# Optimization experiments

Measured on AMD Instinct MI355X. Metric: run time of the kernel, lower is better.

## Reference

```python
import jax, jax.numpy as jnp
import numpy as np
from jax import lax

B, N, C, D = 8, 512, 37, 2048          # frames, rois/frame, classes (incl. bg), feat dim
SCORE_THR = 0.1
NMS_THR = 0.4
BBOX_STDS = np.array([0.1, 0.1, 0.2, 0.2], dtype=np.float32)


def setup_inputs() -> dict:
    key = jax.random.key(0)
    k1, k2, k3, k4, k5, k6 = jax.random.split(key, 6)
    # rois: [batch_idx, x1, y1, x2, y2] in a 600x1000 image
    x1 = jax.random.uniform(k1, (B, N)) * 900.0
    y1 = jax.random.uniform(k2, (B, N)) * 500.0
    w = jax.random.uniform(k3, (B, N)) * 120.0 + 8.0
    h = jax.random.uniform(k4, (B, N)) * 120.0 + 8.0
    bidx = jnp.broadcast_to(jnp.arange(B, dtype=jnp.float32)[:, None], (B, N))
    rois = jnp.stack([bidx, x1, y1, x1 + w, y1 + h], axis=-1)  # [B,N,5]
    bbox_pred = jax.random.normal(k5, (B, N, 4 * C)) * 0.5
    scores = jax.nn.softmax(jax.random.normal(k6, (B, N, C)) * 2.0, axis=-1)
    im_info = jnp.tile(jnp.array([[600.0, 1000.0, 1.0]], dtype=jnp.float32), (B, 1))
    roi_features = jax.random.normal(jax.random.fold_in(key, 7), (B, N, D))
    return {"rois": rois, "bbox_pred": bbox_pred, "scores": scores,
            "im_info": im_info, "roi_features": roi_features}


def _iou_matrix(b):
    # b: [N,4] -> [N,N] pairwise IoU (torchvision nms convention, no +1)
    area = (b[:, 2] - b[:, 0]) * (b[:, 3] - b[:, 1])
    lt = jnp.maximum(b[:, None, :2], b[None, :, :2])
    rb = jnp.minimum(b[:, None, 2:], b[None, :, 2:])
    wh = jnp.clip(rb - lt, 0.0)
    inter = wh[..., 0] * wh[..., 1]
    return inter / (area[:, None] + area[None, :] - inter + 1e-9)


def _nms_one(boxes, scores):
    # boxes [N,4], scores [N] -> keep mask [N] (greedy NMS on score-thresholded boxes)
    n = boxes.shape[0]
    valid = scores > SCORE_THR
    order = jnp.argsort(-jnp.where(valid, scores, -jnp.inf))
    b = boxes[order]
    v = valid[order]
    iou = _iou_matrix(b)
    idx = jnp.arange(n)

    def body(i, keep):
        suppressed = jnp.any((iou[:, i] > NMS_THR) & keep & (idx < i))
        return keep.at[i].set(v[i] & ~suppressed)

    keep_sorted = lax.fori_loop(0, n, body, jnp.zeros(n, bool))
    return jnp.zeros(n, bool).at[order].set(keep_sorted)


def reference(rois, bbox_pred, scores, im_info, roi_features):
    stds = jnp.asarray(BBOX_STDS)
    deltas = bbox_pred.reshape(B, N, C, 4) * stds
    # bbox_transform_inv
    w = (rois[..., 3] - rois[..., 1])[..., None]             # [B,N,1]
    h = (rois[..., 4] - rois[..., 2])[..., None]
    cx = rois[..., 1][..., None] + 0.5 * w
    cy = rois[..., 2][..., None] + 0.5 * h
    px = deltas[..., 0] * w + cx
    py = deltas[..., 1] * h + cy
    pw = jnp.exp(deltas[..., 2]) * w
    ph = jnp.exp(deltas[..., 3]) * h
    x1 = px - 0.5 * pw
    y1 = py - 0.5 * ph
    x2 = px + 0.5 * pw
    y2 = py + 0.5 * ph
    # clip_boxes to image
    xmax = (im_info[:, 1] - 1.0)[:, None, None]
    ymax = (im_info[:, 0] - 1.0)[:, None, None]
    boxes = jnp.stack([jnp.clip(x1, 0.0, xmax), jnp.clip(y1, 0.0, ymax),
                       jnp.clip(x2, 0.0, xmax), jnp.clip(y2, 0.0, ymax)], axis=-1)  # [B,N,C,4]
    # foreground classes 1..C-1, class-major layout: [B,C-1,N,*]
    boxes_fg = jnp.moveaxis(boxes[:, :, 1:, :], 2, 1)        # [B,C-1,N,4]
    scores_fg = jnp.moveaxis(scores[:, :, 1:], 2, 1)         # [B,C-1,N]
    keep = jax.vmap(jax.vmap(_nms_one))(boxes_fg, scores_fg)  # [B,C-1,N] bool
    cls_dets = jnp.where(keep[..., None],
                         jnp.concatenate([boxes_fg, scores_fg[..., None]], axis=-1),
                         0.0)                                 # [B,C-1,N,5]
    kept_feats = jnp.where(jnp.any(keep, axis=1)[..., None], roi_features, 0.0)  # [B,N,D]
    return cls_dets, kept_feats, keep
```

## Files before the change

kernel.cpp:

```cpp
#include <hip/hip_runtime.h>
#include <math.h>

#define BATCH 8
#define BN    512
#define NC    37
#define NFG   36
#define FD    2048
#define NW    2


__global__ __launch_bounds__(128) void nms_kernel(
    const float* __restrict__ rois,
    const float* __restrict__ bbox_pred,
    const float* __restrict__ scores,
    const float* __restrict__ im_info,
    float* __restrict__ cls_dets,
    float* __restrict__ keep_out,
    unsigned char* __restrict__ keep_t)
{
    const int wid  = threadIdx.x >> 6;
    const int lane = threadIdx.x & 63;
    const int bc   = blockIdx.x * NW + wid;
    const int b    = bc / NFG;
    const int cc   = bc % NFG;
    const int c    = cc + 1;

    __shared__ float sb[NW][BN][4];
    __shared__ float sarea[NW][BN];
    __shared__ float cscore[NW][BN];
    __shared__ int   cn[NW][BN];
    __shared__ float kflag[NW][BN];
    __shared__ unsigned char srem[NW][BN];

    const float xmax = im_info[b * 3 + 1] - 1.0f;
    const float ymax = im_info[b * 3 + 0] - 1.0f;
    const unsigned long long lmask_lt = (lane == 0) ? 0ull : ((1ull << lane) - 1ull);

    float  sc[8];
    float4 bp[8];
    float  rx1[8], ry1[8], rx2[8], ry2[8];
#pragma unroll
    for (int r = 0; r < 8; ++r) {
        const int n = r * 64 + lane;
        sc[r] = scores[(size_t)(b * BN + n) * NC + c];
        bp[r] = *(const float4*)(bbox_pred + (size_t)(b * BN + n) * (4 * NC) + 4 * c);
        const float* rr = rois + (size_t)(b * BN + n) * 5;
        rx1[r] = rr[1]; ry1[r] = rr[2]; rx2[r] = rr[3]; ry2[r] = rr[4];
        kflag[wid][n] = 0.0f;
    }

#pragma unroll
    for (int r = 0; r < 8; ++r) {
        const int n = r * 64 + lane;
        const float w  = rx2[r] - rx1[r];
        const float h  = ry2[r] - ry1[r];
        const float cx = rx1[r] + 0.5f * w;
        const float cy = ry1[r] + 0.5f * h;
        const float px = (bp[r].x * 0.1f) * w + cx;
        const float py = (bp[r].y * 0.1f) * h + cy;
        const float pw = expf(bp[r].z * 0.2f) * w;
        const float ph = expf(bp[r].w * 0.2f) * h;
        const float bx1 = fminf(fmaxf(px - 0.5f * pw, 0.0f), xmax);
        const float by1 = fminf(fmaxf(py - 0.5f * ph, 0.0f), ymax);
        const float bx2 = fminf(fmaxf(px + 0.5f * pw, 0.0f), xmax);
        const float by2 = fminf(fmaxf(py + 0.5f * ph, 0.0f), ymax);
        sb[wid][n][0] = bx1; sb[wid][n][1] = by1;
        sb[wid][n][2] = bx2; sb[wid][n][3] = by2;
        sarea[wid][n] = (bx2 - bx1) * (by2 - by1);
    }

    int base = 0;
#pragma unroll
    for (int r = 0; r < 8; ++r) {
        const int n = r * 64 + lane;
        const bool valid = sc[r] > 0.1f;
        const unsigned long long m = __ballot(valid);
        if (valid) {
            const int pos = base + __popcll(m & lmask_lt);
            cscore[wid][pos] = sc[r];
            cn[wid][pos] = n;
        }
        base += __popcll(m);
    }
    const int V = base;
    __builtin_amdgcn_wave_barrier();

    if (V <= 64) {
        float key; int id;
        if (lane < V) { key = cscore[wid][lane]; id = cn[wid][lane]; }
        else          { key = -INFINITY;         id = BN + lane; }
#pragma unroll
        for (int k = 2; k <= 64; k <<= 1) {
#pragma unroll
            for (int j = k >> 1; j > 0; j >>= 1) {
                const float ok = __shfl_xor(key, j);
                const int   oi = __shfl_xor(id, j);
                const bool is_lower   = (lane & j) == 0;
                const bool dir_desc   = (lane & k) == 0;
                const bool mine_first = (key > ok) || (key == ok && id < oi);
                bool take = mine_first ^ is_lower;
                if (!dir_desc) take = !take;
                if (take) { key = ok; id = oi; }
            }
        }
        float x1 = 0, y1 = 0, x2 = 0, y2 = 0, ar = 0;
        if (lane < V) {
            x1 = sb[wid][id][0]; y1 = sb[wid][id][1];
            x2 = sb[wid][id][2]; y2 = sb[wid][id][3];
            ar = sarea[wid][id];
        }
        unsigned long long colmask = 0;
        for (int i = 0; i < V; ++i) {
            const float ax1 = __shfl(x1, i);
            const float ay1 = __shfl(y1, i);
            const float ax2 = __shfl(x2, i);
            const float ay2 = __shfl(y2, i);
            const float aar = __shfl(ar, i);
            const float ix1 = fmaxf(ax1, x1);
            const float iy1 = fmaxf(ay1, y1);
            const float ix2 = fminf(ax2, x2);
            const float iy2 = fminf(ay2, y2);
            const float iw = fmaxf(ix2 - ix1, 0.0f);
            const float ih = fmaxf(iy2 - iy1, 0.0f);
            const float inter = iw * ih;
            const float iou = inter / (aar + ar - inter + 1e-9f);
            if ((iou > 0.4f) && (i < lane)) colmask |= (1ull << i);
        }
        unsigned long long rem = (V == 64) ? ~0ull : ((1ull << V) - 1ull);
        for (int i = 0; i < V; ++i) {
            if (!((rem >> i) & 1ull)) continue;
            rem &= ~__ballot((colmask >> i) & 1ull);
        }
        if (lane < V && ((rem >> lane) & 1ull)) {
            kflag[wid][id] = key;
        }
    } else {
        int P = 64; while (P < V) P <<= 1;
        for (int i = lane; i < P; i += 64) {
            if (i >= V) { cscore[wid][i] = -INFINITY; cn[wid][i] = BN + i; }
            srem[wid][i] = (i < V) ? 1 : 0;
        }
        __builtin_amdgcn_wave_barrier();
        for (int k = 2; k <= P; k <<= 1) {
            for (int j = k >> 1; j > 0; j >>= 1) {
                __builtin_amdgcn_wave_barrier();
                for (int i = lane; i < P; i += 64) {
                    const int ixj = i ^ j;
                    if (ixj > i) {
                        const float ka = cscore[wid][i], kb = cscore[wid][ixj];
                        const int   ia = cn[wid][i],     ib = cn[wid][ixj];
                        const bool a_first = (ka > kb) || (ka == kb && ia < ib);
                        const bool up = ((i & k) == 0);
                        if (up ? !a_first : a_first) {
                            cscore[wid][i] = kb; cscore[wid][ixj] = ka;
                            cn[wid][i] = ib;     cn[wid][ixj] = ia;
                        }
                    }
                }
            }
        }
        __builtin_amdgcn_wave_barrier();
        for (int i = 0; i < V; ++i) {
            __builtin_amdgcn_wave_barrier();
            if (!srem[wid][i]) continue;
            const int   ni  = cn[wid][i];
            const float ax1 = sb[wid][ni][0], ay1 = sb[wid][ni][1];
            const float ax2 = sb[wid][ni][2], ay2 = sb[wid][ni][3];
            const float aar = sarea[wid][ni];
            for (int jj = lane; jj < V; jj += 64) {
                if (jj > i && srem[wid][jj]) {
                    const int nj = cn[wid][jj];
                    const float ix1 = fmaxf(ax1, sb[wid][nj][0]);
                    const float iy1 = fmaxf(ay1, sb[wid][nj][1]);
                    const float ix2 = fminf(ax2, sb[wid][nj][2]);
                    const float iy2 = fminf(ay2, sb[wid][nj][3]);
                    const float iw = fmaxf(ix2 - ix1, 0.0f);
                    const float ih = fmaxf(iy2 - iy1, 0.0f);
                    const float inter = iw * ih;
                    const float iou = inter / (aar + sarea[wid][nj] - inter + 1e-9f);
                    if (iou > 0.4f) srem[wid][jj] = 0;
                }
            }
        }
        __builtin_amdgcn_wave_barrier();
        for (int i = lane; i < V; i += 64) {
            if (srem[wid][i]) kflag[wid][cn[wid][i]] = cscore[wid][i];
        }
    }
    __builtin_amdgcn_wave_barrier();

    const size_t rowbase = (size_t)(b * NFG + cc) * BN;
#pragma unroll
    for (int r = 0; r < 8; ++r) {
        const int n = r * 64 + lane;
        const float s = kflag[wid][n];
        const bool kept = s > 0.0f;
        keep_out[rowbase + n] = kept ? 1.0f : 0.0f;
        keep_t[(size_t)(b * BN + n) * NFG + cc] = kept ? 1 : 0;
        float* cd = cls_dets + (rowbase + n) * 5;
        cd[0] = kept ? sb[wid][n][0] : 0.0f;
        cd[1] = kept ? sb[wid][n][1] : 0.0f;
        cd[2] = kept ? sb[wid][n][2] : 0.0f;
        cd[3] = kept ? sb[wid][n][3] : 0.0f;
        cd[4] = kept ? s : 0.0f;
    }
}

__global__ __launch_bounds__(256) void feat_kernel(
    const float* __restrict__ feats,
    const unsigned char* __restrict__ keep_t,
    float* __restrict__ out_feats)
{
    const int bn = blockIdx.x;

    __shared__ int s_any;
    if (threadIdx.x == 0) s_any = 0;
    __syncthreads();
    if (threadIdx.x < 9) {
        const unsigned int w = *(const unsigned int*)(keep_t + (size_t)bn * NFG
                                                      + 4 * threadIdx.x);
        if (w != 0u) s_any = 1;
    }
    __syncthreads();

    const float4* src = (const float4*)(feats + (size_t)bn * FD);
    float4*       dst = (float4*)(out_feats + (size_t)bn * FD);
    if (s_any) {
#pragma unroll
        for (int t = threadIdx.x; t < FD / 4; t += 256) dst[t] = src[t];
    } else {
        const float4 z = make_float4(0.f, 0.f, 0.f, 0.f);
#pragma unroll
        for (int t = threadIdx.x; t < FD / 4; t += 256) dst[t] = z;
    }
}

extern "C" void kernel_launch(void* const* d_in, const int* in_sizes, int n_in,
                              void* d_out, int out_size, void* d_ws, size_t ws_size,
                              hipStream_t stream) {
    const float* rois      = (const float*)d_in[0];
    const float* bbox_pred = (const float*)d_in[1];
    const float* scores    = (const float*)d_in[2];
    const float* im_info   = (const float*)d_in[3];
    const float* feats     = (const float*)d_in[4];

    float* out        = (float*)d_out;
    float* cls_dets   = out;
    float* kept_feats = out + (size_t)BATCH * NFG * BN * 5;
    float* keep_out   = kept_feats + (size_t)BATCH * BN * FD;

    unsigned char* keep_t = (unsigned char*)d_ws;

    nms_kernel<<<(BATCH * NFG) / NW, 64 * NW, 0, stream>>>(
        rois, bbox_pred, scores, im_info, cls_dets, keep_out, keep_t);
    feat_kernel<<<BATCH * BN, 256, 0, stream>>>(feats, keep_t, kept_feats);
}
```

Measured before the change: 109.0 us.

## Fuse NMS and feature-masking kernels into one cooperative launch with grid sync

Replaces the two-kernel sequence (per-class NMS, then per-ROI feature copy or zero) with a single cooperative kernel. It uses 256 blocks of 4 waves: waves 0..287 run NMS, then a grid-wide sync, then each block masks 16 ROIs' features. This removes a kernel launch and the gap between kernels, and regroups the feature copy into larger per-block chunks. In exchange it pays for a grid barrier and puts the NMS work into fewer, larger blocks, so some blocks sit idle during the NMS phase.

New measurement: 164.9 us. +51.3%, slower.

```diff
diff --git a/kernel.cpp b/kernel.cpp
--- a/kernel.cpp
+++ b/kernel.cpp
@@ -1,237 +1,244 @@
 #include <hip/hip_runtime.h>
+#include <hip/hip_cooperative_groups.h>
 #include <math.h>
+
+namespace cg = cooperative_groups;
 
 #define BATCH 8
 #define BN    512
 #define NC    37
 #define NFG   36
 #define FD    2048
-#define NW    2
-
-
-__global__ __launch_bounds__(128) void nms_kernel(
+#define NWAVE 4
+#define NBLK  256
+#define ROIPB 16
+
+
+__global__ __launch_bounds__(256) void fused_kernel(
     const float* __restrict__ rois,
     const float* __restrict__ bbox_pred,
     const float* __restrict__ scores,
     const float* __restrict__ im_info,
+    const float* __restrict__ feats,
     float* __restrict__ cls_dets,
     float* __restrict__ keep_out,
+    float* __restrict__ out_feats,
     unsigned char* __restrict__ keep_t)
 {
     const int wid  = threadIdx.x >> 6;
     const int lane = threadIdx.x & 63;
-    const int bc   = blockIdx.x * NW + wid;
-    const int b    = bc / NFG;
-    const int cc   = bc % NFG;
-    const int c    = cc + 1;
-
-    __shared__ float sb[NW][BN][4];
-    __shared__ float sarea[NW][BN];
-    __shared__ float cscore[NW][BN];
-    __shared__ int   cn[NW][BN];
-    __shared__ float kflag[NW][BN];
-    __shared__ unsigned char srem[NW][BN];
-
-    const float xmax = im_info[b * 3 + 1] - 1.0f;
-    const float ymax = im_info[b * 3 + 0] - 1.0f;
-    const unsigned long long lmask_lt = (lane == 0) ? 0ull : ((1ull << lane) - 1ull);
-
-    float  sc[8];
-    float4 bp[8];
-    float  rx1[8], ry1[8], rx2[8], ry2[8];
-#pragma unroll
-    for (int r = 0; r < 8; ++r) {
-        const int n = r * 64 + lane;
-        sc[r] = scores[(size_t)(b * BN + n) * NC + c];
-        bp[r] = *(const float4*)(bbox_pred + (size_t)(b * BN + n) * (4 * NC) + 4 * c);
-        const float* rr = rois + (size_t)(b * BN + n) * 5;
-        rx1[r] = rr[1]; ry1[r] = rr[2]; rx2[r] = rr[3]; ry2[r] = rr[4];
-        kflag[wid][n] = 0.0f;
-    }
-
-#pragma unroll
-    for (int r = 0; r < 8; ++r) {
-        const int n = r * 64 + lane;
-        const float w  = rx2[r] - rx1[r];
-        const float h  = ry2[r] - ry1[r];
-        const float cx = rx1[r] + 0.5f * w;
-        const float cy = ry1[r] + 0.5f * h;
-        const float px = (bp[r].x * 0.1f) * w + cx;
-        const float py = (bp[r].y * 0.1f) * h + cy;
-        const float pw = expf(bp[r].z * 0.2f) * w;
-        const float ph = expf(bp[r].w * 0.2f) * h;
-        const float bx1 = fminf(fmaxf(px - 0.5f * pw, 0.0f), xmax);
-        const float by1 = fminf(fmaxf(py - 0.5f * ph, 0.0f), ymax);
-        const float bx2 = fminf(fmaxf(px + 0.5f * pw, 0.0f), xmax);
-        const float by2 = fminf(fmaxf(py + 0.5f * ph, 0.0f), ymax);
-        sb[wid][n][0] = bx1; sb[wid][n][1] = by1;
-        sb[wid][n][2] = bx2; sb[wid][n][3] = by2;
-        sarea[wid][n] = (bx2 - bx1) * (by2 - by1);
-    }
-
-    int base = 0;
-#pragma unroll
-    for (int r = 0; r < 8; ++r) {
-        const int n = r * 64 + lane;
-        const bool valid = sc[r] > 0.1f;
-        const unsigned long long m = __ballot(valid);
-        if (valid) {
-            const int pos = base + __popcll(m & lmask_lt);
-            cscore[wid][pos] = sc[r];
-            cn[wid][pos] = n;
-        }
-        base += __popcll(m);
-    }
-    const int V = base;
-    __builtin_amdgcn_wave_barrier();
-
-    if (V <= 64) {
-        float key; int id;
-        if (lane < V) { key = cscore[wid][lane]; id = cn[wid][lane]; }
-        else          { key = -INFINITY;         id = BN + lane; }
-#pragma unroll
-        for (int k = 2; k <= 64; k <<= 1) {
-#pragma unroll
-            for (int j = k >> 1; j > 0; j >>= 1) {
-                const float ok = __shfl_xor(key, j);
-                const int   oi = __shfl_xor(id, j);
-                const bool is_lower   = (lane & j) == 0;
-                const bool dir_desc   = (lane & k) == 0;
-                const bool mine_first = (key > ok) || (key == ok && id < oi);
-                bool take = mine_first ^ is_lower;
-                if (!dir_desc) take = !take;
-                if (take) { key = ok; id = oi; }
-            }
-        }
-        float x1 = 0, y1 = 0, x2 = 0, y2 = 0, ar = 0;
-        if (lane < V) {
-            x1 = sb[wid][id][0]; y1 = sb[wid][id][1];
-            x2 = sb[wid][id][2]; y2 = sb[wid][id][3];
-            ar = sarea[wid][id];
-        }
-        unsigned long long colmask = 0;
-        for (int i = 0; i < V; ++i) {
-            const float ax1 = __shfl(x1, i);
-            const float ay1 = __shfl(y1, i);
-            const float ax2 = __shfl(x2, i);
-            const float ay2 = __shfl(y2, i);
-            const float aar = __shfl(ar, i);
-            const float ix1 = fmaxf(ax1, x1);
-            const float iy1 = fmaxf(ay1, y1);
-            const float ix2 = fminf(ax2, x2);
-            const float iy2 = fminf(ay2, y2);
-            const float iw = fmaxf(ix2 - ix1, 0.0f);
-            const float ih = fmaxf(iy2 - iy1, 0.0f);
-            const float inter = iw * ih;
-            const float iou = inter / (aar + ar - inter + 1e-9f);
-            if ((iou > 0.4f) && (i < lane)) colmask |= (1ull << i);
-        }
-        unsigned long long rem = (V == 64) ? ~0ull : ((1ull << V) - 1ull);
-        for (int i = 0; i < V; ++i) {
-            if (!((rem >> i) & 1ull)) continue;
-            rem &= ~__ballot((colmask >> i) & 1ull);
-        }
-        if (lane < V && ((rem >> lane) & 1ull)) {
-            kflag[wid][id] = key;
-        }
-    } else {
-        int P = 64; while (P < V) P <<= 1;
-        for (int i = lane; i < P; i += 64) {
-            if (i >= V) { cscore[wid][i] = -INFINITY; cn[wid][i] = BN + i; }
-            srem[wid][i] = (i < V) ? 1 : 0;
-        }
+    const int bc   = blockIdx.x * NWAVE + wid;
+
+    __shared__ float sb[NWAVE][BN][4];
+    __shared__ float sarea[NWAVE][BN];
+    __shared__ float cscore[NWAVE][BN];
+    __shared__ int   cn[NWAVE][BN];
+    __shared__ float kflag[NWAVE][BN];
+    __shared__ unsigned char srem[NWAVE][BN];
+    __shared__ int s_any[ROIPB];
+
+    if (bc < BATCH * NFG) {
+        const int b  = bc / NFG;
+        const int cc = bc % NFG;
+        const int c  = cc + 1;
+
+        const float xmax = im_info[b * 3 + 1] - 1.0f;
+        const float ymax = im_info[b * 3 + 0] - 1.0f;
+        const unsigned long long lmask_lt = (lane == 0) ? 0ull : ((1ull << lane) - 1ull);
+
+        float  sc[8];
+        float4 bp[8];
+        float  rx1[8], ry1[8], rx2[8], ry2[8];
+#pragma unroll
+        for (int r = 0; r < 8; ++r) {
+            const int n = r * 64 + lane;
+            sc[r] = scores[(size_t)(b * BN + n) * NC + c];
+            bp[r] = *(const float4*)(bbox_pred + (size_t)(b * BN + n) * (4 * NC) + 4 * c);
+            const float* rr = rois + (size_t)(b * BN + n) * 5;
+            rx1[r] = rr[1]; ry1[r] = rr[2]; rx2[r] = rr[3]; ry2[r] = rr[4];
+            kflag[wid][n] = 0.0f;
+        }
+
+#pragma unroll
+        for (int r = 0; r < 8; ++r) {
+            const int n = r * 64 + lane;
+            const float w  = rx2[r] - rx1[r];
+            const float h  = ry2[r] - ry1[r];
+            const float cx = rx1[r] + 0.5f * w;
+            const float cy = ry1[r] + 0.5f * h;
+            const float px = (bp[r].x * 0.1f) * w + cx;
+            const float py = (bp[r].y * 0.1f) * h + cy;
+            const float pw = expf(bp[r].z * 0.2f) * w;
+            const float ph = expf(bp[r].w * 0.2f) * h;
+            const float bx1 = fminf(fmaxf(px - 0.5f * pw, 0.0f), xmax);
+            const float by1 = fminf(fmaxf(py - 0.5f * ph, 0.0f), ymax);
+            const float bx2 = fminf(fmaxf(px + 0.5f * pw, 0.0f), xmax);
+            const float by2 = fminf(fmaxf(py + 0.5f * ph, 0.0f), ymax);
+            sb[wid][n][0] = bx1; sb[wid][n][1] = by1;
+            sb[wid][n][2] = bx2; sb[wid][n][3] = by2;
+            sarea[wid][n] = (bx2 - bx1) * (by2 - by1);
+        }
+
+        int base = 0;
+#pragma unroll
+        for (int r = 0; r < 8; ++r) {
+            const int n = r * 64 + lane;
+            const bool valid = sc[r] > 0.1f;
+            const unsigned long long m = __ballot(valid);
+            if (valid) {
+                const int pos = base + __popcll(m & lmask_lt);
+                cscore[wid][pos] = sc[r];
+                cn[wid][pos] = n;
+            }
+            base += __popcll(m);
+        }
+        const int V = base;
         __builtin_amdgcn_wave_barrier();
-        for (int k = 2; k <= P; k <<= 1) {
-            for (int j = k >> 1; j > 0; j >>= 1) {
-                __builtin_amdgcn_wave_barrier();
-                for (int i = lane; i < P; i += 64) {
-                    const int ixj = i ^ j;
-                    if (ixj > i) {
-                        const float ka = cscore[wid][i], kb = cscore[wid][ixj];
-                        const int   ia = cn[wid][i],     ib = cn[wid][ixj];
-                        const bool a_first = (ka > kb) || (ka == kb && ia < ib);
-                        const bool up = ((i & k) == 0);
-                        if (up ? !a_first : a_first) {
-                            cscore[wid][i] = kb; cscore[wid][ixj] = ka;
-                            cn[wid][i] = ib;     cn[wid][ixj] = ia;
+
+        if (V <= 64) {
+            float key; int id;
+            if (lane < V) { key = cscore[wid][lane]; id = cn[wid][lane]; }
+            else          { key = -INFINITY;         id = BN + lane; }
+#pragma unroll
+            for (int k = 2; k <= 64; k <<= 1) {
+#pragma unroll
+                for (int j = k >> 1; j > 0; j >>= 1) {
+                    const float ok = __shfl_xor(key, j);
+                    const int   oi = __shfl_xor(id, j);
+                    const bool is_lower   = (lane & j) == 0;
+                    const bool dir_desc   = (lane & k) == 0;
+                    const bool mine_first = (key > ok) || (key == ok && id < oi);
+                    bool take = mine_first ^ is_lower;
+                    if (!dir_desc) take = !take;
+                    if (take) { key = ok; id = oi; }
+                }
+            }
+            float x1 = 0, y1 = 0, x2 = 0, y2 = 0, ar = 0;
+            if (lane < V) {
+                x1 = sb[wid][id][0]; y1 = sb[wid][id][1];
+                x2 = sb[wid][id][2]; y2 = sb[wid][id][3];
+                ar = sarea[wid][id];
+            }
+            unsigned long long colmask = 0;
+            for (int i = 0; i < V; ++i) {
+                const float ax1 = __shfl(x1, i);
+                const float ay1 = __shfl(y1, i);
+                const float ax2 = __shfl(x2, i);
+                const float ay2 = __shfl(y2, i);
+                const float aar = __shfl(ar, i);
+                const float ix1 = fmaxf(ax1, x1);
+                const float iy1 = fmaxf(ay1, y1);
+                const float ix2 = fminf(ax2, x2);
+                const float iy2 = fminf(ay2, y2);
+                const float iw = fmaxf(ix2 - ix1, 0.0f);
+                const float ih = fmaxf(iy2 - iy1, 0.0f);
+                const float inter = iw * ih;
+                const float iou = inter / (aar + ar - inter + 1e-9f);
+                if ((iou > 0.4f) && (i < lane)) colmask |= (1ull << i);
+            }
+            unsigned long long rem = (V == 64) ? ~0ull : ((1ull << V) - 1ull);
+            for (int i = 0; i < V; ++i) {
+                if (!((rem >> i) & 1ull)) continue;
+                rem &= ~__ballot((colmask >> i) & 1ull);
+            }
+            if (lane < V && ((rem >> lane) & 1ull)) {
+                kflag[wid][id] = key;
+            }
+        } else {
+            int P = 64; while (P < V) P <<= 1;
+            for (int i = lane; i < P; i += 64) {
+                if (i >= V) { cscore[wid][i] = -INFINITY; cn[wid][i] = BN + i; }
+                srem[wid][i] = (i < V) ? 1 : 0;
+            }
+            __builtin_amdgcn_wave_barrier();
+            for (int k = 2; k <= P; k <<= 1) {
+                for (int j = k >> 1; j > 0; j >>= 1) {
+                    __builtin_amdgcn_wave_barrier();
+                    for (int i = lane; i < P; i += 64) {
+                        const int ixj = i ^ j;
+                        if (ixj > i) {
+                            const float ka = cscore[wid][i], kb = cscore[wid][ixj];
+                            const int   ia = cn[wid][i],     ib = cn[wid][ixj];
+                            const bool a_first = (ka > kb) || (ka == kb && ia < ib);
+                            const bool up = ((i & k) == 0);
+                            if (up ? !a_first : a_first) {
+                                cscore[wid][i] = kb; cscore[wid][ixj] = ka;
+                                cn[wid][i] = ib;     cn[wid][ixj] = ia;
+                            }
                         }
                     }
                 }
             }
+            __builtin_amdgcn_wave_barrier();
+            for (int i = 0; i < V; ++i) {
+                __builtin_amdgcn_wave_barrier();
+                if (!srem[wid][i]) continue;
+                const int   ni  = cn[wid][i];
+                const float ax1 = sb[wid][ni][0], ay1 = sb[wid][ni][1];
+                const float ax2 = sb[wid][ni][2], ay2 = sb[wid][ni][3];
+                const float aar = sarea[wid][ni];
+                for (int jj = lane; jj < V; jj += 64) {
+                    if (jj > i && srem[wid][jj]) {
+                        const int nj = cn[wid][jj];
+                        const float ix1 = fmaxf(ax1, sb[wid][nj][0]);
+                        const float iy1 = fmaxf(ay1, sb[wid][nj][1]);
+                        const float ix2 = fminf(ax2, sb[wid][nj][2]);
+                        const float iy2 = fminf(ay2, sb[wid][nj][3]);
+                        const float iw = fmaxf(ix2 - ix1, 0.0f);
+                        const float ih = fmaxf(iy2 - iy1, 0.0f);
+                        const float inter = iw * ih;
+                        const float iou = inter / (aar + sarea[wid][nj] - inter + 1e-9f);
+                        if (iou > 0.4f) srem[wid][jj] = 0;
+                    }
+                }
+            }
+            __builtin_amdgcn_wave_barrier();
+            for (int i = lane; i < V; i += 64) {
+                if (srem[wid][i]) kflag[wid][cn[wid][i]] = cscore[wid][i];
+            }
         }
         __builtin_amdgcn_wave_barrier();
-        for (int i = 0; i < V; ++i) {
-            __builtin_amdgcn_wave_barrier();
-            if (!srem[wid][i]) continue;
-            const int   ni  = cn[wid][i];
-            const float ax1 = sb[wid][ni][0], ay1 = sb[wid][ni][1];
-            const float ax2 = sb[wid][ni][2], ay2 = sb[wid][ni][3];
-            const float aar = sarea[wid][ni];
-            for (int jj = lane; jj < V; jj += 64) {
-                if (jj > i && srem[wid][jj]) {
-                    const int nj = cn[wid][jj];
-                    const float ix1 = fmaxf(ax1, sb[wid][nj][0]);
-                    const float iy1 = fmaxf(ay1, sb[wid][nj][1]);
-                    const float ix2 = fminf(ax2, sb[wid][nj][2]);
-                    const float iy2 = fminf(ay2, sb[wid][nj][3]);
-                    const float iw = fmaxf(ix2 - ix1, 0.0f);
-                    const float ih = fmaxf(iy2 - iy1, 0.0f);
-                    const float inter = iw * ih;
-                    const float iou = inter / (aar + sarea[wid][nj] - inter + 1e-9f);
-                    if (iou > 0.4f) srem[wid][jj] = 0;
-                }
-            }
-        }
-        __builtin_amdgcn_wave_barrier();
-        for (int i = lane; i < V; i += 64) {
-            if (srem[wid][i]) kflag[wid][cn[wid][i]] = cscore[wid][i];
+
+        const size_t rowbase = (size_t)(b * NFG + cc) * BN;
+#pragma unroll
+        for (int r = 0; r < 8; ++r) {
+            const int n = r * 64 + lane;
+            const float s = kflag[wid][n];
+            const bool kept = s > 0.0f;
+            keep_out[rowbase + n] = kept ? 1.0f : 0.0f;
+            keep_t[(size_t)(b * BN + n) * NFG + cc] = kept ? 1 : 0;
+            float* cd = cls_dets + (rowbase + n) * 5;
+            cd[0] = kept ? sb[wid][n][0] : 0.0f;
+            cd[1] = kept ? sb[wid][n][1] : 0.0f;
+            cd[2] = kept ? sb[wid][n][2] : 0.0f;
+            cd[3] = kept ? sb[wid][n][3] : 0.0f;
+            cd[4] = kept ? s : 0.0f;
         }
     }
-    __builtin_amdgcn_wave_barrier();
-
-    const size_t rowbase = (size_t)(b * NFG + cc) * BN;
-#pragma unroll
-    for (int r = 0; r < 8; ++r) {
-        const int n = r * 64 + lane;
-        const float s = kflag[wid][n];
-        const bool kept = s > 0.0f;
-        keep_out[rowbase + n] = kept ? 1.0f : 0.0f;
-        keep_t[(size_t)(b * BN + n) * NFG + cc] = kept ? 1 : 0;
-        float* cd = cls_dets + (rowbase + n) * 5;
-        cd[0] = kept ? sb[wid][n][0] : 0.0f;
-        cd[1] = kept ? sb[wid][n][1] : 0.0f;
-        cd[2] = kept ? sb[wid][n][2] : 0.0f;
-        cd[3] = kept ? sb[wid][n][3] : 0.0f;
-        cd[4] = kept ? s : 0.0f;
-    }
-}
-
-__global__ __launch_bounds__(256) void feat_kernel(
-    const float* __restrict__ feats,
-    const unsigned char* __restrict__ keep_t,
-    float* __restrict__ out_feats)
-{
-    const int bn = blockIdx.x;
-
-    __shared__ int s_any;
-    if (threadIdx.x == 0) s_any = 0;
+
+    cg::this_grid().sync();
+
+    if (threadIdx.x < ROIPB) s_any[threadIdx.x] = 0;
     __syncthreads();
-    if (threadIdx.x < 9) {
-        const unsigned int w = *(const unsigned int*)(keep_t + (size_t)bn * NFG
-                                                      + 4 * threadIdx.x);
-        if (w != 0u) s_any = 1;
+    if (threadIdx.x < ROIPB * 9) {
+        const int rl = threadIdx.x / 9;
+        const int dw = threadIdx.x % 9;
+        const int roi = blockIdx.x * ROIPB + rl;
+        const unsigned int w = *(const unsigned int*)(keep_t + (size_t)roi * NFG + 4 * dw);
+        if (w != 0u) atomicOr(&s_any[rl], 1);
     }
     __syncthreads();
 
-    const float4* src = (const float4*)(feats + (size_t)bn * FD);
-    float4*       dst = (float4*)(out_feats + (size_t)bn * FD);
-    if (s_any) {
-#pragma unroll
-        for (int t = threadIdx.x; t < FD / 4; t += 256) dst[t] = src[t];
-    } else {
-        const float4 z = make_float4(0.f, 0.f, 0.f, 0.f);
-#pragma unroll
-        for (int t = threadIdx.x; t < FD / 4; t += 256) dst[t] = z;
+    const size_t fbase = (size_t)blockIdx.x * ROIPB * FD;
+    const float4* src = (const float4*)(feats + fbase);
+    float4*       dst = (float4*)(out_feats + fbase);
+    const float4 z = make_float4(0.f, 0.f, 0.f, 0.f);
+#pragma unroll
+    for (int i = 0; i < (ROIPB * FD / 4) / 256; ++i) {
+        const int idx = i * 256 + threadIdx.x;
+        const int rl  = i >> 1;
+        if (s_any[rl]) dst[idx] = src[idx];
+        else           dst[idx] = z;
     }
 }
 
@@ -251,7 +258,11 @@
 
     unsigned char* keep_t = (unsigned char*)d_ws;
 
-    nms_kernel<<<(BATCH * NFG) / NW, 64 * NW, 0, stream>>>(
-        rois, bbox_pred, scores, im_info, cls_dets, keep_out, keep_t);
-    feat_kernel<<<BATCH * BN, 256, 0, stream>>>(feats, keep_t, kept_feats);
+    void* args[] = {
+        (void*)&rois, (void*)&bbox_pred, (void*)&scores, (void*)&im_info,
+        (void*)&feats, (void*)&cls_dets, (void*)&keep_out, (void*)&kept_feats,
+        (void*)&keep_t
+    };
+    hipLaunchCooperativeKernel((const void*)fused_kernel, dim3(NBLK), dim3(256),
+                               args, 0, stream);
 }
```
